# Performance work log

Hardware: AMD Instinct MI355X
Metric: run time of the kernel (lower is better)

## Reference

```python
import jax, jax.numpy as jnp
import numpy as np

NUM_HEADS = 32
KV_HEADS = 8
HEAD_DIM = 64
HIDDEN = 2048
ROPE_THETA = 10000.0


def setup_inputs() -> dict:
    key = jax.random.key(0)
    ks = jax.random.split(key, 5)
    B, S, H = 2, 2048, HIDDEN
    scale = 0.02
    return {
        "x": jax.random.normal(ks[0], (B, S, H), dtype=jnp.float32),
        # weights stored as (in_features, out_features)
        "Wq": jax.random.normal(ks[1], (H, NUM_HEADS * HEAD_DIM), dtype=jnp.float32) * scale,
        "Wk": jax.random.normal(ks[2], (H, KV_HEADS * HEAD_DIM), dtype=jnp.float32) * scale,
        "Wv": jax.random.normal(ks[3], (H, KV_HEADS * HEAD_DIM), dtype=jnp.float32) * scale,
        "Wo": jax.random.normal(ks[4], (H, H), dtype=jnp.float32) * scale,
    }


def _rope_tables(seq_len, dtype):
    # freq over even dims, angles concatenated twice -> (S, HEAD_DIM)
    freq = 1.0 / (ROPE_THETA ** (jnp.arange(0, HEAD_DIM, 2, dtype=jnp.float32) / HEAD_DIM))
    ang = jnp.arange(seq_len, dtype=jnp.float32)[:, None] * freq[None, :]
    emb = jnp.concatenate([ang, ang], axis=-1)
    return jnp.cos(emb).astype(dtype), jnp.sin(emb).astype(dtype)


def _rotate_half(x):
    x1, x2 = jnp.split(x, 2, axis=-1)
    return jnp.concatenate([-x2, x1], axis=-1)


def reference(x, Wq, Wk, Wv, Wo):
    B, S, H = x.shape
    q = jnp.einsum("bsd,df->bsf", x, Wq).reshape(B, S, NUM_HEADS, HEAD_DIM).transpose(0, 2, 1, 3)
    k = jnp.einsum("bsd,df->bsf", x, Wk).reshape(B, S, KV_HEADS, HEAD_DIM).transpose(0, 2, 1, 3)
    v = jnp.einsum("bsd,df->bsf", x, Wv).reshape(B, S, KV_HEADS, HEAD_DIM).transpose(0, 2, 1, 3)

    cos, sin = _rope_tables(S, x.dtype)  # (S, HEAD_DIM), broadcasts over (B, h, S, D)
    q = q * cos + _rotate_half(q) * sin
    k = k * cos + _rotate_half(k) * sin

    n_rep = NUM_HEADS // KV_HEADS
    k = jnp.repeat(k, n_rep, axis=1)  # (B, NUM_HEADS, S, D)
    v = jnp.repeat(v, n_rep, axis=1)

    scores = jnp.einsum("bhsd,bhtd->bhst", q, k) / jnp.sqrt(jnp.asarray(HEAD_DIM, x.dtype))
    weights = jax.nn.softmax(scores, axis=-1)
    ctx = jnp.einsum("bhst,bhtd->bhsd", weights, v)
    ctx = ctx.transpose(0, 2, 1, 3).reshape(B, S, H)
    return jnp.einsum("bsd,df->bsf", ctx, Wo)
```

## Files before the change

### kernel.cpp

```cpp
#include <hip/hip_runtime.h>

typedef short s8v __attribute__((ext_vector_type(8)));
typedef int i2v __attribute__((ext_vector_type(2)));
typedef float f2v __attribute__((ext_vector_type(2)));
typedef float f4v __attribute__((ext_vector_type(4)));

typedef const __attribute__((address_space(1))) char* gp1_t;
typedef __attribute__((address_space(3))) char* lp3_t;

__device__ __forceinline__ float bf2f(short s) {
    union { unsigned u; float f; } c;
    c.u = ((unsigned)(unsigned short)s) << 16;
    return c.f;
}
__device__ __forceinline__ short f2bf(float f) {
    union { float f; unsigned u; } c; c.f = f;
    unsigned r = (c.u + 0x7FFFu + ((c.u >> 16) & 1u)) >> 16;
    return (short)r;
}
__device__ __forceinline__ unsigned cvt_pk_bf16(float a, float b) {
    unsigned r;
    asm("v_cvt_pk_bf16_f32 %0, %1, %2" : "=v"(r) : "v"(a), "v"(b));
    return r;
}
__device__ __forceinline__ s8v cvt8(const float* __restrict__ p) {
    f4v a = *(const f4v*)p;
    f4v b = *(const f4v*)(p + 4);
    s8v r;
    r[0] = f2bf(a[0]); r[1] = f2bf(a[1]); r[2] = f2bf(a[2]); r[3] = f2bf(a[3]);
    r[4] = f2bf(b[0]); r[5] = f2bf(b[1]); r[6] = f2bf(b[2]); r[7] = f2bf(b[3]);
    return r;
}


__global__ __launch_bounds__(256) void cvt_x(const float* __restrict__ x,
                                             short* __restrict__ xb) {
    long i = ((long)blockIdx.x * 256 + threadIdx.x) * 8;
    *(s8v*)&xb[i] = cvt8(&x[i]);
}

__global__ __launch_bounds__(256) void cvt_wt(const float* __restrict__ W,
                                              short* __restrict__ Wt,
                                              int N, int obase, float scale) {
    __shared__ __align__(16) short tile[64 * 72];
    const int kt = blockIdx.y * 64, n0 = blockIdx.x * 64;
    const int t = threadIdx.x;
    const int r = t >> 4, c4 = (t & 15) * 4;
#pragma unroll
    for (int i = 0; i < 4; i++) {
        int kr = r + i * 16;
        f4v v = *(const f4v*)&W[(long)(kt + kr) * N + n0 + c4];
#pragma unroll
        for (int j = 0; j < 4; j++) tile[(c4 + j) * 72 + kr] = f2bf(v[j] * scale);
    }
    __syncthreads();
    const int nr = t >> 3, kc = (t & 7) * 8;
#pragma unroll
    for (int i = 0; i < 2; i++) {
        int n = nr + i * 32;
        *(s8v*)&Wt[(long)(obase + n0 + n) * 2048 + kt + kc] = *(const s8v*)&tile[n * 72 + kc];
    }
}

template <bool CF32>
__global__ __launch_bounds__(256) void gemm_bt(const short* __restrict__ A,
                                               const short* __restrict__ Bt,
                                               void* __restrict__ Cv,
                                               int K, int lda, int ldb, int ldc) {
    __shared__ __align__(16) short As[128 * 32];
    __shared__ __align__(16) short Bs[128 * 32];
    const int tid = threadIdx.x;
    const int lane = tid & 63;
    const int wave = tid >> 6;
    const int quad = lane >> 4;
    const int l15 = lane & 15;

    const int nwg = gridDim.x * gridDim.y;
    int f = blockIdx.y * gridDim.x + blockIdx.x;
    if ((nwg & 7) == 0) f = (f & 7) * (nwg >> 3) + (f >> 3);
    const int m0 = (f / gridDim.x) * 128;
    const int n0 = (f % gridDim.x) * 128;

    const int wm = (wave & 1) * 64;
    const int wn = (wave >> 1) * 64;

    f4v acc[4][4];
#pragma unroll
    for (int i = 0; i < 4; i++)
#pragma unroll
        for (int j = 0; j < 4; j++) acc[i][j] = (f4v){0.f, 0.f, 0.f, 0.f};

    const int s0 = wave * 64 + lane, s1 = (4 + wave) * 64 + lane;
    const short* a0 = A + (long)(m0 + (s0 >> 2)) * lda + (s0 & 3) * 8;
    const short* a1 = A + (long)(m0 + (s1 >> 2)) * lda + (s1 & 3) * 8;
    const short* b0 = Bt + (long)(n0 + (s0 >> 2)) * ldb + (s0 & 3) * 8;
    const short* b1 = Bt + (long)(n0 + (s1 >> 2)) * ldb + (s1 & 3) * 8;
    char* lA0 = (char*)As + wave * 1024;
    char* lA1 = (char*)As + (4 + wave) * 1024;
    char* lB0 = (char*)Bs + wave * 1024;
    char* lB1 = (char*)Bs + (4 + wave) * 1024;

    for (int k0 = 0; k0 < K; k0 += 32) {
        __syncthreads();
        __builtin_amdgcn_global_load_lds((gp1_t)(a0 + k0), (lp3_t)lA0, 16, 0, 0);
        __builtin_amdgcn_global_load_lds((gp1_t)(a1 + k0), (lp3_t)lA1, 16, 0, 0);
        __builtin_amdgcn_global_load_lds((gp1_t)(b0 + k0), (lp3_t)lB0, 16, 0, 0);
        __builtin_amdgcn_global_load_lds((gp1_t)(b1 + k0), (lp3_t)lB1, 16, 0, 0);
        __syncthreads();
        s8v af[4], bfr[4];
#pragma unroll
        for (int mi = 0; mi < 4; mi++)
            af[mi] = *(const s8v*)(&As[(wm + mi * 16 + l15) * 32 + quad * 8]);
#pragma unroll
        for (int ni = 0; ni < 4; ni++)
            bfr[ni] = *(const s8v*)(&Bs[(wn + ni * 16 + l15) * 32 + quad * 8]);
#pragma unroll
        for (int mi = 0; mi < 4; mi++)
#pragma unroll
            for (int ni = 0; ni < 4; ni++)
                acc[mi][ni] = __builtin_amdgcn_mfma_f32_16x16x32_bf16(af[mi], bfr[ni], acc[mi][ni], 0, 0, 0);
    }
#pragma unroll
    for (int mi = 0; mi < 4; mi++)
#pragma unroll
        for (int ni = 0; ni < 4; ni++)
#pragma unroll
            for (int r = 0; r < 4; r++) {
                int row = m0 + wm + mi * 16 + quad * 4 + r;
                int col = n0 + wn + ni * 16 + l15;
                if (CF32) ((float*)Cv)[(long)row * ldc + col] = acc[mi][ni][r];
                else      ((short*)Cv)[(long)row * ldc + col] = f2bf(acc[mi][ni][r]);
            }
}

__global__ __launch_bounds__(256) void rope_kernel(short* __restrict__ qkv) {
    int tid = blockIdx.x * 256 + threadIdx.x;
    int p = tid % 1280;
    int row = tid / 1280;
    int head = p >> 5;
    int j = p & 31;
    int s = row & 2047;
    int c1 = head * 64 + j;
    float freq = exp2f(-(float)j * 0.4152410118609203f);
    float ang = (float)s * freq;
    float sn, cs;
    __sincosf(ang, &sn, &cs);
    long base = (long)row * 3072;
    float x1 = bf2f(qkv[base + c1]);
    float x2 = bf2f(qkv[base + c1 + 32]);
    qkv[base + c1]      = f2bf(x1 * cs - x2 * sn);
    qkv[base + c1 + 32] = f2bf(x2 * cs + x1 * sn);
}

__global__ __launch_bounds__(256) void vtrans(const short* __restrict__ qkv,
                                              short* __restrict__ Vt_g) {
    __shared__ __align__(16) short tile[64 * 72];
    const int kt = blockIdx.x * 64;
    const int kvh = blockIdx.y;
    const int b = blockIdx.z;
    const int t = threadIdx.x;
#pragma unroll
    for (int cc = 0; cc < 2; cc++) {
        int ch = t + cc * 256;
        int key = ch >> 3, d0 = (ch & 7) * 8;
        s8v v = *(const s8v*)&qkv[(long)(b * 2048 + kt + key) * 3072 + 2560 + kvh * 64 + d0];
#pragma unroll
        for (int i = 0; i < 8; i++) tile[(d0 + i) * 72 + key] = v[i];
    }
    __syncthreads();
#pragma unroll
    for (int cc = 0; cc < 2; cc++) {
        int ch = t + cc * 256;
        int d = ch >> 3, kc = (ch & 7) * 8;
        *(s8v*)&Vt_g[(long)((b * 8 + kvh) * 64 + d) * 2048 + kt + kc] = *(const s8v*)&tile[d * 72 + kc];
    }
}

__global__ __launch_bounds__(256, 3) void attn4(short* __restrict__ qkv,
                                                const short* __restrict__ Vt_g) {
    __shared__ __align__(16) short KV[2][2][4096];
    __shared__ __align__(16) short Ps[4][2][16 * 72];
    __shared__ float rsb[4][32];

    const int tid = threadIdx.x;
    const int lane = tid & 63;
    const int wave = tid >> 6;
    const int quad = lane >> 4;
    const int l15 = lane & 15;

    int f = (blockIdx.z * 32 + blockIdx.y) * 16 + blockIdx.x;
    f = (f & 7) * 128 + (f >> 3);
    const int b = f >> 9;
    const int h = (f >> 4) & 31;
    const int kvh = h >> 2;
    const int q0 = (f & 15) * 128;

    const long kbase = ((long)b * 2048) * 3072 + 2048 + kvh * 64;
    const long vtbase = (long)(b * 8 + kvh) * 64 * 2048;

    const long qrow = (long)b * 2048 + q0 + wave * 32 + l15;
    const short* qp = qkv + qrow * 3072 + h * 64 + quad * 8;
    const s8v qf00 = *(const s8v*)(qp);
    const s8v qf01 = *(const s8v*)(qp + 32);
    const s8v qf10 = *(const s8v*)(qp + 16 * 3072);
    const s8v qf11 = *(const s8v*)(qp + 16 * 3072 + 32);

    const int rA = wave * 8 + (lane >> 3);
    const int sslot = (lane & 7) ^ (lane >> 3);
    const short* kA = qkv + kbase + (long)rA * 3072 + sslot * 8;
    const short* kB = kA + (long)32 * 3072;
    const short* vA = Vt_g + vtbase + (long)rA * 2048 + sslot * 8;
    const short* vB = vA + (long)32 * 2048;

    {
        char* kd = (char*)&KV[0][0][0] + wave * 1024;
        char* vd = (char*)&KV[0][1][0] + wave * 1024;
        __builtin_amdgcn_global_load_lds((gp1_t)kA, (lp3_t)kd, 16, 0, 0);
        __builtin_amdgcn_global_load_lds((gp1_t)kB, (lp3_t)(kd + 4096), 16, 0, 0);
        __builtin_amdgcn_global_load_lds((gp1_t)vA, (lp3_t)vd, 16, 0, 0);
        __builtin_amdgcn_global_load_lds((gp1_t)vB, (lp3_t)(vd + 4096), 16, 0, 0);
    }
    __syncthreads();

    const int ks0 = ((quad ^ (l15 & 7)) << 3);
    const int ks1 = ks0 ^ 32;

    f2v rs0v = (f2v){0.f, 0.f}, rs1v = (f2v){0.f, 0.f};
    f4v o0[4], o1[4];
#pragma unroll
    for (int ni = 0; ni < 4; ni++) { o0[ni] = (f4v){0.f, 0.f, 0.f, 0.f}; o1[ni] = (f4v){0.f, 0.f, 0.f, 0.f}; }

    short* Pw0 = &Ps[wave][0][0];
    short* Pw1 = &Ps[wave][1][0];

    for (int t = 0; t < 32; ++t) {
        const short* Kb = &KV[t & 1][0][0];
        const short* Vb = &KV[t & 1][1][0];

        if (t < 31) {
            const long ko = (long)(t + 1) * (64 * 3072);
            const long vo = (long)(t + 1) * 64;
            char* kd = (char*)&KV[(t + 1) & 1][0][0] + wave * 1024;
            char* vd = (char*)&KV[(t + 1) & 1][1][0] + wave * 1024;
            __builtin_amdgcn_global_load_lds((gp1_t)(kA + ko), (lp3_t)kd, 16, 0, 0);
            __builtin_amdgcn_global_load_lds((gp1_t)(kB + ko), (lp3_t)(kd + 4096), 16, 0, 0);
            __builtin_amdgcn_global_load_lds((gp1_t)(vA + vo), (lp3_t)vd, 16, 0, 0);
            __builtin_amdgcn_global_load_lds((gp1_t)(vB + vo), (lp3_t)(vd + 4096), 16, 0, 0);
        }

#pragma unroll
        for (int ni = 0; ni < 4; ni++) {
            const int ro = (ni * 16 + l15) * 64;
            const s8v kf0 = *(const s8v*)&Kb[ro + ks0];
            const s8v kf1 = *(const s8v*)&Kb[ro + ks1];
            f4v a = (f4v){-24.f, -24.f, -24.f, -24.f};
            a = __builtin_amdgcn_mfma_f32_16x16x32_bf16(kf0, qf00, a, 0, 0, 0);
            a = __builtin_amdgcn_mfma_f32_16x16x32_bf16(kf1, qf01, a, 0, 0, 0);
            {
                float p0 = exp2f(a[0]);
                float p1 = exp2f(a[1]);
                float p2 = exp2f(a[2]);
                float p3 = exp2f(a[3]);
                rs0v += (f2v){p0, p1};
                rs0v += (f2v){p2, p3};
                *(i2v*)&Pw0[l15 * 72 + ni * 16 + quad * 4] =
                    (i2v){(int)cvt_pk_bf16(p0, p1), (int)cvt_pk_bf16(p2, p3)};
            }
            f4v c = (f4v){-24.f, -24.f, -24.f, -24.f};
            c = __builtin_amdgcn_mfma_f32_16x16x32_bf16(kf0, qf10, c, 0, 0, 0);
            c = __builtin_amdgcn_mfma_f32_16x16x32_bf16(kf1, qf11, c, 0, 0, 0);
            {
                float p0 = exp2f(c[0]);
                float p1 = exp2f(c[1]);
                float p2 = exp2f(c[2]);
                float p3 = exp2f(c[3]);
                rs1v += (f2v){p0, p1};
                rs1v += (f2v){p2, p3};
                *(i2v*)&Pw1[l15 * 72 + ni * 16 + quad * 4] =
                    (i2v){(int)cvt_pk_bf16(p0, p1), (int)cvt_pk_bf16(p2, p3)};
            }
        }

        const s8v pf00 = *(const s8v*)&Pw0[l15 * 72 + quad * 8];
        const s8v pf01 = *(const s8v*)&Pw0[l15 * 72 + 32 + quad * 8];
        const s8v pf10 = *(const s8v*)&Pw1[l15 * 72 + quad * 8];
        const s8v pf11 = *(const s8v*)&Pw1[l15 * 72 + 32 + quad * 8];
#pragma unroll
        for (int ni = 0; ni < 4; ni++) {
            const int ro = (ni * 16 + l15) * 64;
            const s8v vf0 = *(const s8v*)&Vb[ro + ks0];
            const s8v vf1 = *(const s8v*)&Vb[ro + ks1];
            o0[ni] = __builtin_amdgcn_mfma_f32_16x16x32_bf16(pf00, vf0, o0[ni], 0, 0, 0);
            o0[ni] = __builtin_amdgcn_mfma_f32_16x16x32_bf16(pf01, vf1, o0[ni], 0, 0, 0);
            o1[ni] = __builtin_amdgcn_mfma_f32_16x16x32_bf16(pf10, vf0, o1[ni], 0, 0, 0);
            o1[ni] = __builtin_amdgcn_mfma_f32_16x16x32_bf16(pf11, vf1, o1[ni], 0, 0, 0);
        }
        __syncthreads();
    }

    float rs0 = rs0v[0] + rs0v[1];
    float rs1 = rs1v[0] + rs1v[1];
    rs0 += __shfl_xor(rs0, 16); rs0 += __shfl_xor(rs0, 32);
    rs1 += __shfl_xor(rs1, 16); rs1 += __shfl_xor(rs1, 32);
    if (quad == 0) { rsb[wave][l15] = rs0; rsb[wave][16 + l15] = rs1; }
    __syncthreads();

#pragma unroll
    for (int r = 0; r < 4; r++) {
        const float i0 = 1.0f / rsb[wave][quad * 4 + r];
        const float i1 = 1.0f / rsb[wave][16 + quad * 4 + r];
        const long ob0 = ((long)b * 2048 + q0 + wave * 32 + quad * 4 + r) * 3072 + h * 64;
        const long ob1 = ob0 + 16 * 3072;
#pragma unroll
        for (int ni = 0; ni < 4; ni++) {
            qkv[ob0 + ni * 16 + l15] = f2bf(o0[ni][r] * i0);
            qkv[ob1 + ni * 16 + l15] = f2bf(o1[ni][r] * i1);
        }
    }
}


template <bool AF32, bool CF32>
__global__ __launch_bounds__(256) void gemm_bn(const void* __restrict__ Av,
                                               const float* __restrict__ B,
                                               void* __restrict__ Cv,
                                               int K, int N, int lda, int ldc) {
    __shared__ __align__(16) short As[128 * 40];
    __shared__ __align__(16) short Bs[128 * 40];
    const int tid = threadIdx.x;
    const int lane = tid & 63;
    const int wave = tid >> 6;
    const int quad = lane >> 4;
    const int l15 = lane & 15;
    const int m0 = blockIdx.y * 128;
    const int n0 = blockIdx.x * 128;
    const int wm = (wave & 1) * 64;
    const int wn = (wave >> 1) * 64;

    f4v acc[4][4];
#pragma unroll
    for (int i = 0; i < 4; i++)
#pragma unroll
        for (int j = 0; j < 4; j++) acc[i][j] = (f4v){0.f, 0.f, 0.f, 0.f};

    const int ar0 = tid >> 2, akc0 = (tid & 3) * 8;
    const int ar1 = (tid + 256) >> 2, akc1 = ((tid + 256) & 3) * 8;
    const int bk0 = tid >> 4, bnc0 = (tid & 15) * 8;
    const int bk1 = (tid + 256) >> 4, bnc1 = ((tid + 256) & 15) * 8;

    for (int k0 = 0; k0 < K; k0 += 32) {
        __syncthreads();
        if (AF32) {
            const float* A = (const float*)Av;
            *(s8v*)(&As[ar0 * 40 + akc0]) = cvt8(&A[(long)(m0 + ar0) * lda + k0 + akc0]);
            *(s8v*)(&As[ar1 * 40 + akc1]) = cvt8(&A[(long)(m0 + ar1) * lda + k0 + akc1]);
        } else {
            const short* A = (const short*)Av;
            *(s8v*)(&As[ar0 * 40 + akc0]) = *(const s8v*)(&A[(long)(m0 + ar0) * lda + k0 + akc0]);
            *(s8v*)(&As[ar1 * 40 + akc1]) = *(const s8v*)(&A[(long)(m0 + ar1) * lda + k0 + akc1]);
        }
        s8v b0 = cvt8(&B[(long)(k0 + bk0) * N + n0 + bnc0]);
        s8v b1 = cvt8(&B[(long)(k0 + bk1) * N + n0 + bnc1]);
#pragma unroll
        for (int i = 0; i < 8; i++) Bs[(bnc0 + i) * 40 + bk0] = b0[i];
#pragma unroll
        for (int i = 0; i < 8; i++) Bs[(bnc1 + i) * 40 + bk1] = b1[i];
        __syncthreads();
        s8v af[4], bfr[4];
#pragma unroll
        for (int mi = 0; mi < 4; mi++)
            af[mi] = *(const s8v*)(&As[(wm + mi * 16 + l15) * 40 + quad * 8]);
#pragma unroll
        for (int ni = 0; ni < 4; ni++)
            bfr[ni] = *(const s8v*)(&Bs[(wn + ni * 16 + l15) * 40 + quad * 8]);
#pragma unroll
        for (int mi = 0; mi < 4; mi++)
#pragma unroll
            for (int ni = 0; ni < 4; ni++)
                acc[mi][ni] = __builtin_amdgcn_mfma_f32_16x16x32_bf16(af[mi], bfr[ni], acc[mi][ni], 0, 0, 0);
    }
#pragma unroll
    for (int mi = 0; mi < 4; mi++)
#pragma unroll
        for (int ni = 0; ni < 4; ni++)
#pragma unroll
            for (int r = 0; r < 4; r++) {
                int row = m0 + wm + mi * 16 + quad * 4 + r;
                int col = n0 + wn + ni * 16 + l15;
                if (CF32) ((float*)Cv)[(long)row * ldc + col] = acc[mi][ni][r];
                else      ((short*)Cv)[(long)row * ldc + col] = f2bf(acc[mi][ni][r]);
            }
}

__global__ __launch_bounds__(256) void attn_kernel(short* __restrict__ qkv) {
    __shared__ __align__(16) short Qs[64 * 72];
    __shared__ __align__(16) short Ks[64 * 72];
    __shared__ __align__(16) short Vt[64 * 72];
    __shared__ __align__(16) short Ps[4][16 * 72];

    const int tid = threadIdx.x;
    const int lane = tid & 63;
    const int wave = tid >> 6;
    const int quad = lane >> 4;
    const int l15 = lane & 15;
    const int b = blockIdx.z;
    const int h = blockIdx.y;
    const int kvh = h >> 2;
    const int q0 = blockIdx.x * 64;

    const long qbase = ((long)b * 2048 + q0) * 3072 + h * 64;
    const long kbase = ((long)b * 2048) * 3072 + 2048 + kvh * 64;
    const long vbase = kbase + 512;

#pragma unroll
    for (int cc = 0; cc < 2; cc++) {
        int ch = tid + cc * 256;
        int r = ch >> 3, d0 = (ch & 7) * 8;
        *(s8v*)(&Qs[r * 72 + d0]) = *(const s8v*)(&qkv[qbase + (long)r * 3072 + d0]);
    }
    __syncthreads();
    s8v qf[2];
    qf[0] = *(const s8v*)(&Qs[(wave * 16 + l15) * 72 + quad * 8]);
    qf[1] = *(const s8v*)(&Qs[(wave * 16 + l15) * 72 + 32 + quad * 8]);

    float m_i[4], l_i[4];
    f4v o[4];
#pragma unroll
    for (int r = 0; r < 4; r++) { m_i[r] = -1e30f; l_i[r] = 0.0f; }
#pragma unroll
    for (int ni = 0; ni < 4; ni++) o[ni] = (f4v){0.f, 0.f, 0.f, 0.f};

    for (int kt = 0; kt < 2048; kt += 64) {
        __syncthreads();
#pragma unroll
        for (int cc = 0; cc < 2; cc++) {
            int ch = tid + cc * 256;
            int r = ch >> 3, d0 = (ch & 7) * 8;
            *(s8v*)(&Ks[r * 72 + d0]) = *(const s8v*)(&qkv[kbase + (long)(kt + r) * 3072 + d0]);
            s8v v = *(const s8v*)(&qkv[vbase + (long)(kt + r) * 3072 + d0]);
            int g = d0 >> 3;
            int chn = ((r >> 3) ^ g) * 8 + (r & 7);
#pragma unroll
            for (int i = 0; i < 8; i++) Vt[(d0 + i) * 72 + chn] = v[i];
        }
        __syncthreads();

        f4v sc[4];
#pragma unroll
        for (int ni = 0; ni < 4; ni++) {
            s8v kf0 = *(const s8v*)(&Ks[(ni * 16 + l15) * 72 + quad * 8]);
            s8v kf1 = *(const s8v*)(&Ks[(ni * 16 + l15) * 72 + 32 + quad * 8]);
            f4v a = (f4v){0.f, 0.f, 0.f, 0.f};
            a = __builtin_amdgcn_mfma_f32_16x16x32_bf16(qf[0], kf0, a, 0, 0, 0);
            a = __builtin_amdgcn_mfma_f32_16x16x32_bf16(qf[1], kf1, a, 0, 0, 0);
            sc[ni] = a * 0.125f;
        }
        float alpha[4], rs[4];
#pragma unroll
        for (int r = 0; r < 4; r++) {
            float v = fmaxf(fmaxf(sc[0][r], sc[1][r]), fmaxf(sc[2][r], sc[3][r]));
            v = fmaxf(v, __shfl_xor(v, 1));
            v = fmaxf(v, __shfl_xor(v, 2));
            v = fmaxf(v, __shfl_xor(v, 4));
            v = fmaxf(v, __shfl_xor(v, 8));
            float mn = fmaxf(m_i[r], v);
            alpha[r] = __expf(m_i[r] - mn);
            m_i[r] = mn;
            rs[r] = 0.f;
        }
#pragma unroll
        for (int ni = 0; ni < 4; ni++)
#pragma unroll
            for (int r = 0; r < 4; r++) {
                float pv = __expf(sc[ni][r] - m_i[r]);
                sc[ni][r] = pv;
                rs[r] += pv;
            }
#pragma unroll
        for (int r = 0; r < 4; r++) {
            float v = rs[r];
            v += __shfl_xor(v, 1);
            v += __shfl_xor(v, 2);
            v += __shfl_xor(v, 4);
            v += __shfl_xor(v, 8);
            l_i[r] = l_i[r] * alpha[r] + v;
        }
#pragma unroll
        for (int ni = 0; ni < 4; ni++)
#pragma unroll
            for (int r = 0; r < 4; r++) {
                int row = quad * 4 + r;
                int key = ni * 16 + l15;
                int chn = ((key >> 3) ^ (row >> 3)) * 8 + (key & 7);
                Ps[wave][row * 72 + chn] = f2bf(sc[ni][r]);
            }
        __syncthreads();
#pragma unroll
        for (int ni = 0; ni < 4; ni++) {
            f4v t = o[ni];
            t[0] *= alpha[0]; t[1] *= alpha[1]; t[2] *= alpha[2]; t[3] *= alpha[3];
            o[ni] = t;
        }
        s8v pf0 = *(const s8v*)(&Ps[wave][l15 * 72 + ((quad ^ (l15 >> 3)) * 8)]);
        s8v pf1 = *(const s8v*)(&Ps[wave][l15 * 72 + (((4 + quad) ^ (l15 >> 3)) * 8)]);
#pragma unroll
        for (int ni = 0; ni < 4; ni++) {
            int d = ni * 16 + l15;
            s8v vf0 = *(const s8v*)(&Vt[d * 72 + ((quad ^ (d >> 3)) * 8)]);
            s8v vf1 = *(const s8v*)(&Vt[d * 72 + (((4 + quad) ^ (d >> 3)) * 8)]);
            o[ni] = __builtin_amdgcn_mfma_f32_16x16x32_bf16(pf0, vf0, o[ni], 0, 0, 0);
            o[ni] = __builtin_amdgcn_mfma_f32_16x16x32_bf16(pf1, vf1, o[ni], 0, 0, 0);
        }
    }
#pragma unroll
    for (int r = 0; r < 4; r++) {
        float inv = 1.0f / l_i[r];
        int srow = q0 + wave * 16 + quad * 4 + r;
        long obase = ((long)b * 2048 + srow) * 3072 + h * 64;
#pragma unroll
        for (int ni = 0; ni < 4; ni++)
            qkv[obase + ni * 16 + l15] = f2bf(o[ni][r] * inv);
    }
}

extern "C" void kernel_launch(void* const* d_in, const int* in_sizes, int n_in,
                              void* d_out, int out_size, void* d_ws, size_t ws_size,
                              hipStream_t stream) {
    (void)in_sizes; (void)n_in; (void)out_size;
    const float* x  = (const float*)d_in[0];
    const float* Wq = (const float*)d_in[1];
    const float* Wk = (const float*)d_in[2];
    const float* Wv = (const float*)d_in[3];
    const float* Wo = (const float*)d_in[4];

    const float CS = 0.18033688011112042f;
    const size_t need = 67108864ULL;
    if (ws_size >= need) {
        short* xb    = (short*)d_ws;
        short* Wqkvt = xb + 8388608;
        short* Wot   = Wqkvt + 6291456;
        short* qkv   = Wot + 4194304;
        short* Vt_g  = qkv + 12582912;

        cvt_x<<<4096, 256, 0, stream>>>(x, xb);
        cvt_wt<<<dim3(32, 32), 256, 0, stream>>>(Wq, Wqkvt, 2048, 0, 1.0f);
        cvt_wt<<<dim3(8, 32), 256, 0, stream>>>(Wk, Wqkvt, 512, 2048, CS);
        cvt_wt<<<dim3(8, 32), 256, 0, stream>>>(Wv, Wqkvt, 512, 2560, 1.0f);
        cvt_wt<<<dim3(32, 32), 256, 0, stream>>>(Wo, Wot, 2048, 0, 1.0f);
        gemm_bt<false><<<dim3(24, 32), 256, 0, stream>>>(xb, Wqkvt, qkv, 2048, 2048, 2048, 3072);
        rope_kernel<<<dim3(20480), 256, 0, stream>>>(qkv);
        vtrans<<<dim3(32, 8, 2), 256, 0, stream>>>(qkv, Vt_g);
        attn4<<<dim3(16, 32, 2), 256, 0, stream>>>(qkv, Vt_g);
        gemm_bt<true><<<dim3(16, 32), 256, 0, stream>>>(qkv, Wot, d_out, 2048, 3072, 2048, 2048);
    } else {
        short* qkv = (short*)d_ws;
        gemm_bn<true, false><<<dim3(16, 32), 256, 0, stream>>>(x, Wq, qkv,        2048, 2048, 2048, 3072);
        gemm_bn<true, false><<<dim3(4, 32), 256, 0, stream>>>(x, Wk, qkv + 2048, 2048,  512, 2048, 3072);
        gemm_bn<true, false><<<dim3(4, 32), 256, 0, stream>>>(x, Wv, qkv + 2560, 2048,  512, 2048, 3072);
        rope_kernel<<<dim3(20480), 256, 0, stream>>>(qkv);
        attn_kernel<<<dim3(32, 32, 2), 256, 0, stream>>>(qkv);
        gemm_bn<false, true><<<dim3(16, 32), 256, 0, stream>>>(qkv, Wo, d_out, 2048, 2048, 3072, 2048);
    }
}
```

Baseline: 364.7 us.

## Replace bf16 GEMM with 256x256 tile, 8-wave double-buffered pipelined kernel

The 128x128, 4-wave GEMM used for the QKV and output projections is replaced by a 256x256-tile, 8-wave kernel. It double-buffers K=64 slices in LDS with a swizzled layout and issues global-to-LDS loads for upcoming slices in between the MFMA phases, using setprio and partial vmcnt waits. The aim is to raise arithmetic intensity per block, hide global load latency and avoid LDS bank conflicts. In exchange it uses much more LDS per block (128KB) and far fewer blocks (192 and 128), which may underfill the 256 CUs.

```diff
diff --git a/kernel.cpp b/kernel.cpp
--- a/kernel.cpp
+++ b/kernel.cpp
@@ -63,12 +63,13 @@
 }
 
 template <bool CF32>
-__global__ __launch_bounds__(256) void gemm_bt(const short* __restrict__ A,
-                                               const short* __restrict__ Bt,
-                                               void* __restrict__ Cv,
-                                               int K, int lda, int ldb, int ldc) {
-    __shared__ __align__(16) short As[128 * 32];
-    __shared__ __align__(16) short Bs[128 * 32];
+__global__ __launch_bounds__(512, 2) void gemm_bt8(const short* __restrict__ A,
+                                                   const short* __restrict__ Bt,
+                                                   void* __restrict__ Cv,
+                                                   int K, int lda, int ldb, int ldc) {
+    __shared__ __align__(16) short Ab[2][16384];
+    __shared__ __align__(16) short Bb[2][16384];
+
     const int tid = threadIdx.x;
     const int lane = tid & 63;
     const int wave = tid >> 6;
@@ -78,59 +79,154 @@
     const int nwg = gridDim.x * gridDim.y;
     int f = blockIdx.y * gridDim.x + blockIdx.x;
     if ((nwg & 7) == 0) f = (f & 7) * (nwg >> 3) + (f >> 3);
-    const int m0 = (f / gridDim.x) * 128;
-    const int n0 = (f % gridDim.x) * 128;
-
-    const int wm = (wave & 1) * 64;
-    const int wn = (wave >> 1) * 64;
-
-    f4v acc[4][4];
-#pragma unroll
-    for (int i = 0; i < 4; i++)
-#pragma unroll
-        for (int j = 0; j < 4; j++) acc[i][j] = (f4v){0.f, 0.f, 0.f, 0.f};
-
-    const int s0 = wave * 64 + lane, s1 = (4 + wave) * 64 + lane;
-    const short* a0 = A + (long)(m0 + (s0 >> 2)) * lda + (s0 & 3) * 8;
-    const short* a1 = A + (long)(m0 + (s1 >> 2)) * lda + (s1 & 3) * 8;
-    const short* b0 = Bt + (long)(n0 + (s0 >> 2)) * ldb + (s0 & 3) * 8;
-    const short* b1 = Bt + (long)(n0 + (s1 >> 2)) * ldb + (s1 & 3) * 8;
-    char* lA0 = (char*)As + wave * 1024;
-    char* lA1 = (char*)As + (4 + wave) * 1024;
-    char* lB0 = (char*)Bs + wave * 1024;
-    char* lB1 = (char*)Bs + (4 + wave) * 1024;
-
-    for (int k0 = 0; k0 < K; k0 += 32) {
-        __syncthreads();
-        __builtin_amdgcn_global_load_lds((gp1_t)(a0 + k0), (lp3_t)lA0, 16, 0, 0);
-        __builtin_amdgcn_global_load_lds((gp1_t)(a1 + k0), (lp3_t)lA1, 16, 0, 0);
-        __builtin_amdgcn_global_load_lds((gp1_t)(b0 + k0), (lp3_t)lB0, 16, 0, 0);
-        __builtin_amdgcn_global_load_lds((gp1_t)(b1 + k0), (lp3_t)lB1, 16, 0, 0);
-        __syncthreads();
-        s8v af[4], bfr[4];
+    const int m0 = (f / gridDim.x) * 256;
+    const int n0 = (f % gridDim.x) * 256;
+
+    const int wm = (wave >> 2) * 128;
+    const int wn = (wave & 3) * 64;
+
+    const int rsub = lane >> 3;
+    const int sslot = (lane & 7) ^ rsub;
+    const short* aS[2][2];
+    const short* bS[2][2];
+#pragma unroll
+    for (int h = 0; h < 2; h++)
+#pragma unroll
+        for (int i = 0; i < 2; i++) {
+            int row = h * 128 + wave * 16 + i * 8 + rsub;
+            aS[h][i] = A  + (long)(m0 + row) * lda + sslot * 8;
+            bS[h][i] = Bt + (long)(n0 + row) * ldb + sslot * 8;
+        }
+
+    auto stageA = [&](int buf, int h, int kt) {
+        char* d = (char*)&Ab[buf][0] + h * 16384 + wave * 2048;
+        __builtin_amdgcn_global_load_lds((gp1_t)(aS[h][0] + (long)kt * 64), (lp3_t)d, 16, 0, 0);
+        __builtin_amdgcn_global_load_lds((gp1_t)(aS[h][1] + (long)kt * 64), (lp3_t)(d + 1024), 16, 0, 0);
+    };
+    auto stageB = [&](int buf, int h, int kt) {
+        char* d = (char*)&Bb[buf][0] + h * 16384 + wave * 2048;
+        __builtin_amdgcn_global_load_lds((gp1_t)(bS[h][0] + (long)kt * 64), (lp3_t)d, 16, 0, 0);
+        __builtin_amdgcn_global_load_lds((gp1_t)(bS[h][1] + (long)kt * 64), (lp3_t)(d + 1024), 16, 0, 0);
+    };
+
+    const int ks0 = (quad ^ (l15 & 7)) * 8;
+    const int ks1 = ks0 ^ 32;
+
+    f4v acc[2][4][2][2];
+#pragma unroll
+    for (int a = 0; a < 2; a++)
+#pragma unroll
+        for (int b = 0; b < 4; b++)
+#pragma unroll
+            for (int c = 0; c < 2; c++)
+#pragma unroll
+                for (int d = 0; d < 2; d++) acc[a][b][c][d] = (f4v){0.f, 0.f, 0.f, 0.f};
+
+    const int NT = K >> 6;
+
+    stageB(0, 0, 0); stageB(0, 1, 0); stageA(0, 0, 0); stageA(0, 1, 0);
+    stageB(1, 0, 1); stageB(1, 1, 1); stageA(1, 0, 1);
+    asm volatile("s_waitcnt vmcnt(6)" ::: "memory");
+    __builtin_amdgcn_s_barrier();
+
+    for (int t = 0; t < NT; ++t) {
+        const short* Ac = &Ab[t & 1][0];
+        const short* Bc = &Bb[t & 1][0];
+        const int nb = (t + 1) & 1;
+        s8v af[4][2], bf0[2][2], bf1[2][2];
+
+#pragma unroll
+        for (int mi = 0; mi < 4; mi++) {
+            const int row = wm + mi * 16 + l15;
+            af[mi][0] = *(const s8v*)&Ac[row * 64 + ks0];
+            af[mi][1] = *(const s8v*)&Ac[row * 64 + ks1];
+        }
+#pragma unroll
+        for (int ni = 0; ni < 2; ni++) {
+            const int row = wn + ni * 16 + l15;
+            bf0[ni][0] = *(const s8v*)&Bc[row * 64 + ks0];
+            bf0[ni][1] = *(const s8v*)&Bc[row * 64 + ks1];
+        }
+        if (t + 1 < NT) stageA(nb, 1, t + 1);
+        __builtin_amdgcn_s_setprio(1);
 #pragma unroll
         for (int mi = 0; mi < 4; mi++)
-            af[mi] = *(const s8v*)(&As[(wm + mi * 16 + l15) * 32 + quad * 8]);
-#pragma unroll
-        for (int ni = 0; ni < 4; ni++)
-            bfr[ni] = *(const s8v*)(&Bs[(wn + ni * 16 + l15) * 32 + quad * 8]);
+#pragma unroll
+            for (int ni = 0; ni < 2; ni++) {
+                acc[0][mi][0][ni] = __builtin_amdgcn_mfma_f32_16x16x32_bf16(af[mi][0], bf0[ni][0], acc[0][mi][0][ni], 0, 0, 0);
+                acc[0][mi][0][ni] = __builtin_amdgcn_mfma_f32_16x16x32_bf16(af[mi][1], bf0[ni][1], acc[0][mi][0][ni], 0, 0, 0);
+            }
+        __builtin_amdgcn_s_setprio(0);
+        __builtin_amdgcn_s_barrier();
+
+#pragma unroll
+        for (int ni = 0; ni < 2; ni++) {
+            const int row = wn + 32 + ni * 16 + l15;
+            bf1[ni][0] = *(const s8v*)&Bc[row * 64 + ks0];
+            bf1[ni][1] = *(const s8v*)&Bc[row * 64 + ks1];
+        }
+        __builtin_amdgcn_s_setprio(1);
 #pragma unroll
         for (int mi = 0; mi < 4; mi++)
 #pragma unroll
-            for (int ni = 0; ni < 4; ni++)
-                acc[mi][ni] = __builtin_amdgcn_mfma_f32_16x16x32_bf16(af[mi], bfr[ni], acc[mi][ni], 0, 0, 0);
-    }
-#pragma unroll
-    for (int mi = 0; mi < 4; mi++)
-#pragma unroll
-        for (int ni = 0; ni < 4; ni++)
-#pragma unroll
-            for (int r = 0; r < 4; r++) {
-                int row = m0 + wm + mi * 16 + quad * 4 + r;
-                int col = n0 + wn + ni * 16 + l15;
-                if (CF32) ((float*)Cv)[(long)row * ldc + col] = acc[mi][ni][r];
-                else      ((short*)Cv)[(long)row * ldc + col] = f2bf(acc[mi][ni][r]);
-            }
+            for (int ni = 0; ni < 2; ni++) {
+                acc[0][mi][1][ni] = __builtin_amdgcn_mfma_f32_16x16x32_bf16(af[mi][0], bf1[ni][0], acc[0][mi][1][ni], 0, 0, 0);
+                acc[0][mi][1][ni] = __builtin_amdgcn_mfma_f32_16x16x32_bf16(af[mi][1], bf1[ni][1], acc[0][mi][1][ni], 0, 0, 0);
+            }
+        __builtin_amdgcn_s_setprio(0);
+        __builtin_amdgcn_s_barrier();
+
+#pragma unroll
+        for (int mi = 0; mi < 4; mi++) {
+            const int row = wm + 64 + mi * 16 + l15;
+            af[mi][0] = *(const s8v*)&Ac[row * 64 + ks0];
+            af[mi][1] = *(const s8v*)&Ac[row * 64 + ks1];
+        }
+        if (t + 2 < NT) stageB(t & 1, 0, t + 2);
+        __builtin_amdgcn_s_setprio(1);
+#pragma unroll
+        for (int mi = 0; mi < 4; mi++)
+#pragma unroll
+            for (int ni = 0; ni < 2; ni++) {
+                acc[1][mi][0][ni] = __builtin_amdgcn_mfma_f32_16x16x32_bf16(af[mi][0], bf0[ni][0], acc[1][mi][0][ni], 0, 0, 0);
+                acc[1][mi][0][ni] = __builtin_amdgcn_mfma_f32_16x16x32_bf16(af[mi][1], bf0[ni][1], acc[1][mi][0][ni], 0, 0, 0);
+            }
+        __builtin_amdgcn_s_setprio(0);
+        __builtin_amdgcn_s_barrier();
+
+        if (t + 2 < NT) { stageB(t & 1, 1, t + 2); stageA(t & 1, 0, t + 2); }
+        __builtin_amdgcn_s_setprio(1);
+#pragma unroll
+        for (int mi = 0; mi < 4; mi++)
+#pragma unroll
+            for (int ni = 0; ni < 2; ni++) {
+                acc[1][mi][1][ni] = __builtin_amdgcn_mfma_f32_16x16x32_bf16(af[mi][0], bf1[ni][0], acc[1][mi][1][ni], 0, 0, 0);
+                acc[1][mi][1][ni] = __builtin_amdgcn_mfma_f32_16x16x32_bf16(af[mi][1], bf1[ni][1], acc[1][mi][1][ni], 0, 0, 0);
+            }
+        __builtin_amdgcn_s_setprio(0);
+        if (t + 1 < NT) {
+            if (t + 1 == NT - 1) asm volatile("s_waitcnt vmcnt(0)" ::: "memory");
+            else                 asm volatile("s_waitcnt vmcnt(6)" ::: "memory");
+            __builtin_amdgcn_s_barrier();
+        }
+    }
+
+#pragma unroll
+    for (int qm = 0; qm < 2; qm++)
+#pragma unroll
+        for (int mi = 0; mi < 4; mi++)
+#pragma unroll
+            for (int qn = 0; qn < 2; qn++)
+#pragma unroll
+                for (int ni = 0; ni < 2; ni++)
+#pragma unroll
+                    for (int r = 0; r < 4; r++) {
+                        int row = m0 + wm + qm * 64 + mi * 16 + quad * 4 + r;
+                        int col = n0 + wn + qn * 32 + ni * 16 + l15;
+                        float v = acc[qm][mi][qn][ni][r];
+                        if (CF32) ((float*)Cv)[(long)row * ldc + col] = v;
+                        else      ((short*)Cv)[(long)row * ldc + col] = f2bf(v);
+                    }
 }
 
 __global__ __launch_bounds__(256) void rope_kernel(short* __restrict__ qkv) {
@@ -547,11 +643,11 @@
         cvt_wt<<<dim3(8, 32), 256, 0, stream>>>(Wk, Wqkvt, 512, 2048, CS);
         cvt_wt<<<dim3(8, 32), 256, 0, stream>>>(Wv, Wqkvt, 512, 2560, 1.0f);
         cvt_wt<<<dim3(32, 32), 256, 0, stream>>>(Wo, Wot, 2048, 0, 1.0f);
-        gemm_bt<false><<<dim3(24, 32), 256, 0, stream>>>(xb, Wqkvt, qkv, 2048, 2048, 2048, 3072);
+        gemm_bt8<false><<<dim3(12, 16), 512, 0, stream>>>(xb, Wqkvt, qkv, 2048, 2048, 2048, 3072);
         rope_kernel<<<dim3(20480), 256, 0, stream>>>(qkv);
         vtrans<<<dim3(32, 8, 2), 256, 0, stream>>>(qkv, Vt_g);
         attn4<<<dim3(16, 32, 2), 256, 0, stream>>>(qkv, Vt_g);
-        gemm_bt<true><<<dim3(16, 32), 256, 0, stream>>>(qkv, Wot, d_out, 2048, 3072, 2048, 2048);
+        gemm_bt8<true><<<dim3(8, 16), 512, 0, stream>>>(qkv, Wot, d_out, 2048, 3072, 2048, 2048);
     } else {
         short* qkv = (short*)d_ws;
         gemm_bn<true, false><<<dim3(16, 32), 256, 0, stream>>>(x, Wq, qkv,        2048, 2048, 2048, 3072);
```

New measurement: 357.3 us. 2.0% less time.
